# Kernel tuning notes

Measured on AMD Instinct MI355X. Metric: run time of the kernel, lower is better.

## Reference

```python
import jax, jax.numpy as jnp
import numpy as np

NUM_HEADS = 4
EMBED_DIM = 256
HEAD_DIM = EMBED_DIM // NUM_HEADS
B, N = 4, 4096


def setup_inputs() -> dict:
    key = jax.random.key(0)
    kq, kk, kv, kw = jax.random.split(key, 4)
    q = jax.random.normal(kq, (B, N, EMBED_DIM), dtype=jnp.float32)
    k = jax.random.normal(kk, (B, N, EMBED_DIM), dtype=jnp.float32)
    v = jax.random.normal(kv, (B, N, EMBED_DIM), dtype=jnp.float32)
    W_out = jax.random.normal(kw, (EMBED_DIM, EMBED_DIM), dtype=jnp.float32) * (1.0 / np.sqrt(EMBED_DIM))
    b_out = jnp.zeros((EMBED_DIM,), dtype=jnp.float32)
    return {"q": q, "k": k, "v": v, "W_out": W_out, "b_out": b_out}


def reference(q, k, v, W_out, b_out):
    b, n, _ = q.shape
    # [b, n, e] -> [b, h, n, d]
    qh = q.reshape(b, n, NUM_HEADS, HEAD_DIM).transpose(0, 2, 1, 3)
    kh = k.reshape(b, n, NUM_HEADS, HEAD_DIM).transpose(0, 2, 1, 3)
    vh = v.reshape(b, n, NUM_HEADS, HEAD_DIM).transpose(0, 2, 1, 3)
    scale = 1.0 / jnp.sqrt(jnp.asarray(HEAD_DIM, dtype=qh.dtype))
    # full [b, h, n, n] score matrix, as in the original module
    attn = jnp.einsum('bhqd,bhkd->bhqk', qh, kh) * scale
    attn = jax.nn.softmax(attn, axis=-1)
    out = jnp.einsum('bhqk,bhkd->bhqd', attn, vh)
    out = out.transpose(0, 2, 1, 3).reshape(b, n, EMBED_DIM)
    # nn.Linear: x @ W.T + b
    return out @ W_out.T + b_out
```

## Files before the change

### kernel.cpp

```cpp
#include <hip/hip_runtime.h>
#include <hip/hip_bf16.h>

#define B_ 4
#define H_ 4
#define N_ 4096
#define D_ 64
#define E_ 256
#define KVB 64
#define QBLK 256
#define NT (N_ / KVB)

typedef short short8 __attribute__((ext_vector_type(8)));
typedef float f32x4 __attribute__((ext_vector_type(4)));
typedef float f32x16 __attribute__((ext_vector_type(16)));

__device__ __forceinline__ ushort f2bf(float f) {
  union { float f; unsigned u; } a; a.f = f;
  unsigned r = a.u + 0x7fffu + ((a.u >> 16) & 1u);
  return (ushort)(r >> 16);
}

__device__ __forceinline__ unsigned cvt_pk_bf16(float lo, float hi) {
  unsigned r;
  asm("v_cvt_pk_bf16_f32 %0, %1, %2" : "=v"(r) : "v"(lo), "v"(hi));
  return r;
}

__device__ __forceinline__ void permlane32_swap(unsigned &a, unsigned &b) {
  asm volatile("v_permlane32_swap_b32 %0, %1" : "+v"(a), "+v"(b));
}

__global__ void cast_w_kernel(const float* __restrict__ W, ushort* __restrict__ Wb) {
  int i = blockIdx.x * blockDim.x + threadIdx.x;
  float4 x = ((const float4*)W)[i];
  ushort4 o;
  o.x = f2bf(x.x); o.y = f2bf(x.y); o.z = f2bf(x.z); o.w = f2bf(x.w);
  ((ushort4*)Wb)[i] = o;
}

__global__ void prep_kv(const float* __restrict__ k, const float* __restrict__ v,
                        ushort* __restrict__ Kb, ushort* __restrict__ Vtb) {
  __shared__ float vt[64][65];
  const int gid = blockIdx.x;
  const int bh = gid >> 6, t = gid & 63;
  const int b = bh >> 2, h = bh & 3;
  const int tid = threadIdx.x;
  const int rr = tid >> 4, cc = (tid & 15) * 4;
  const float* kg = k + ((size_t)b * N_ + t * 64) * E_ + h * 64;
  const float* vg = v + ((size_t)b * N_ + t * 64) * E_ + h * 64;
  ushort* ko = Kb + (size_t)gid * 4096;
  ushort* vo = Vtb + (size_t)gid * 4096;
  for (int it = 0; it < 4; ++it) {
    int r = rr + it * 16;
    float4 kx = *(const float4*)(kg + (size_t)r * E_ + cc);
    float4 vx = *(const float4*)(vg + (size_t)r * E_ + cc);
    uint2 kp;
    kp.x = (unsigned)f2bf(kx.x) | ((unsigned)f2bf(kx.y) << 16);
    kp.y = (unsigned)f2bf(kx.z) | ((unsigned)f2bf(kx.w) << 16);
    *(uint2*)(ko + r * 64 + cc) = kp;
    vt[r][cc] = vx.x; vt[r][cc + 1] = vx.y; vt[r][cc + 2] = vx.z; vt[r][cc + 3] = vx.w;
  }
  __syncthreads();
  for (int it = 0; it < 4; ++it) {
    int dr = rr + it * 16;
    uint2 vp;
    vp.x = (unsigned)f2bf(vt[cc][dr]) | ((unsigned)f2bf(vt[cc + 1][dr]) << 16);
    vp.y = (unsigned)f2bf(vt[cc + 2][dr]) | ((unsigned)f2bf(vt[cc + 3][dr]) << 16);
    *(uint2*)(vo + dr * 64 + cc) = vp;
  }
}

__launch_bounds__(512, 2)
__global__ void attn_kernel(const float* __restrict__ q,
                            const ushort* __restrict__ Kb,
                            const ushort* __restrict__ Vtb,
                            ushort* __restrict__ X) {
  __shared__ __attribute__((aligned(16))) ushort Ks[2][4096];
  __shared__ __attribute__((aligned(16))) ushort Vs[2][4096];
  __shared__ float Lb[8][32];

  const int bid = blockIdx.x;
  const int swz = (bid & 7) * 32 + (bid >> 3);
  const int bh = swz >> 4;
  const int qt = swz & 15;
  const int b = bh >> 2, h = bh & 3;
  const int tid = threadIdx.x;
  const int wid = tid >> 6;
  const int lane = tid & 63;
  const int ln = lane & 31;
  const int hi = lane >> 5;

  const int off = tid * 16;
  const int sw = (off & ~127) | ((off & 127) ^ (((off >> 7) & 7) << 4));
  const char* Kg = (const char*)Kb + (size_t)bh * NT * 8192;
  const char* Vg = (const char*)Vtb + (size_t)bh * NT * 8192;

  const float SC = 0.125f * 1.44269504f;
  const int qrow0 = qt * QBLK + wid * 32;
  const float* Qg = q + ((size_t)b * N_ + qrow0 + ln) * E_ + h * D_;
  short8 qf[4];
#pragma unroll
  for (int ks = 0; ks < 4; ++ks) {
    const float* p = Qg + ks * 16 + hi * 8;
    float4 x0 = *(const float4*)(p);
    float4 x1 = *(const float4*)(p + 4);
    short8 f;
    f[0] = (short)f2bf(x0.x * SC); f[1] = (short)f2bf(x0.y * SC);
    f[2] = (short)f2bf(x0.z * SC); f[3] = (short)f2bf(x0.w * SC);
    f[4] = (short)f2bf(x1.x * SC); f[5] = (short)f2bf(x1.y * SC);
    f[6] = (short)f2bf(x1.z * SC); f[7] = (short)f2bf(x1.w * SC);
    qf[ks] = f;
  }

  f32x16 O0 = (f32x16)0.0f, O1 = (f32x16)0.0f;
  float lsum = 0.f;

  {
    uint4 k0 = *(const uint4*)(Kg + off);
    uint4 v0 = *(const uint4*)(Vg + off);
    *(uint4*)((char*)Ks[0] + sw) = k0;
    *(uint4*)((char*)Vs[0] + sw) = v0;
  }
  __syncthreads();
  int cur = 0;

  for (int t = 0; t < NT; ++t) {
    const bool pfn = (t + 1 < NT);
    uint4 rk, rv;
    if (pfn) {
      rk = *(const uint4*)(Kg + (size_t)(t + 1) * 8192 + off);
      rv = *(const uint4*)(Vg + (size_t)(t + 1) * 8192 + off);
    }

    short8 kf[2][4];
#pragma unroll
    for (int nb = 0; nb < 2; ++nb)
#pragma unroll
      for (int ks = 0; ks < 4; ++ks) {
        int kvr = nb * 32 + ln;
        kf[nb][ks] = *(short8*)((char*)Ks[cur] + kvr * 128 +
                                ((ks * 32 + hi * 16) ^ ((kvr & 7) << 4)));
      }

    f32x16 S0 = (f32x16)0.0f, S1 = (f32x16)0.0f;
#pragma unroll
    for (int ks = 0; ks < 4; ++ks) {
      S0 = __builtin_amdgcn_mfma_f32_32x32x16_bf16(kf[0][ks], qf[ks], S0, 0, 0, 0);
      S1 = __builtin_amdgcn_mfma_f32_32x32x16_bf16(kf[1][ks], qf[ks], S1, 0, 0, 0);
    }

    float p[32];
#pragma unroll
    for (int i = 0; i < 16; ++i) {
      p[i]      = __builtin_amdgcn_exp2f(S0[i]);
      p[16 + i] = __builtin_amdgcn_exp2f(S1[i]);
    }
    float ls = 0.f;
#pragma unroll
    for (int i = 0; i < 32; ++i) ls += p[i];
    lsum += ls;

    short8 pa[4];
#pragma unroll
    for (int nb = 0; nb < 2; ++nb)
#pragma unroll
      for (int ksp = 0; ksp < 2; ++ksp) {
        int base = nb * 16 + ksp * 8;
        unsigned w0 = cvt_pk_bf16(p[base + 0], p[base + 1]);
        unsigned w2 = cvt_pk_bf16(p[base + 4], p[base + 5]);
        permlane32_swap(w0, w2);
        unsigned w1 = cvt_pk_bf16(p[base + 2], p[base + 3]);
        unsigned w3 = cvt_pk_bf16(p[base + 6], p[base + 7]);
        permlane32_swap(w1, w3);
        uint4 u; u.x = w0; u.y = w1; u.z = w2; u.w = w3;
        union { uint4 u4; short8 s8; } cv; cv.u4 = u;
        pa[nb * 2 + ksp] = cv.s8;
      }

    if (pfn) {
      *(uint4*)((char*)Ks[cur ^ 1] + sw) = rk;
      *(uint4*)((char*)Vs[cur ^ 1] + sw) = rv;
    }

    short8 vf[2][4];
#pragma unroll
    for (int db = 0; db < 2; ++db)
#pragma unroll
      for (int ks = 0; ks < 4; ++ks) {
        int d = db * 32 + ln;
        vf[db][ks] = *(short8*)((char*)Vs[cur] + d * 128 +
                                ((ks * 32 + hi * 16) ^ ((d & 7) << 4)));
      }

#pragma unroll
    for (int ks = 0; ks < 4; ++ks) {
      O0 = __builtin_amdgcn_mfma_f32_32x32x16_bf16(pa[ks], vf[0][ks], O0, 0, 0, 0);
      O1 = __builtin_amdgcn_mfma_f32_32x32x16_bf16(pa[ks], vf[1][ks], O1, 0, 0, 0);
    }

    __syncthreads();
    cur ^= 1;
  }

  float l = lsum + __shfl_xor(lsum, 32);
  if (lane < 32) Lb[wid][lane] = l;
  asm volatile("" ::: "memory");
  float inv[16];
#pragma unroll
  for (int r = 0; r < 16; ++r)
    inv[r] = 1.0f / Lb[wid][(r & 3) + 8 * (r >> 2) + 4 * hi];

  ushort* Xp = X + ((size_t)b * N_) * E_ + h * D_;
#pragma unroll
  for (int r = 0; r < 16; ++r) {
    int qrow = qrow0 + (r & 3) + 8 * (r >> 2) + 4 * hi;
    Xp[(size_t)qrow * E_ + ln]      = f2bf(O0[r] * inv[r]);
    Xp[(size_t)qrow * E_ + 32 + ln] = f2bf(O1[r] * inv[r]);
  }
}

__launch_bounds__(256, 2)
__global__ void proj_kernel(const ushort* __restrict__ X, const ushort* __restrict__ Wb,
                            const float* __restrict__ bias, float* __restrict__ out) {
  const int m0   = blockIdx.x * 64;
  const int tid  = threadIdx.x;
  const int wid  = tid >> 6;
  const int lane = tid & 63;
  const int g    = lane >> 4;
  const int lr   = lane & 15;
  const int n0   = wid * 64;

  f32x4 acc[4][4];
  for (int mb = 0; mb < 4; ++mb)
    for (int nb = 0; nb < 4; ++nb)
      acc[mb][nb] = (f32x4){0.f, 0.f, 0.f, 0.f};

  for (int k0 = 0; k0 < E_; k0 += 32) {
    short8 af[4], bfr[4];
    for (int mb = 0; mb < 4; ++mb)
      af[mb] = *(const short8*)(X + (size_t)(m0 + mb * 16 + lr) * E_ + k0 + g * 8);
    for (int nb = 0; nb < 4; ++nb)
      bfr[nb] = *(const short8*)(Wb + (size_t)(n0 + nb * 16 + lr) * E_ + k0 + g * 8);
    for (int mb = 0; mb < 4; ++mb)
      for (int nb = 0; nb < 4; ++nb)
        acc[mb][nb] = __builtin_amdgcn_mfma_f32_16x16x32_bf16(af[mb], bfr[nb], acc[mb][nb], 0, 0, 0);
  }

  for (int nb = 0; nb < 4; ++nb) {
    float bv = bias[n0 + nb * 16 + lr];
    for (int mb = 0; mb < 4; ++mb)
      for (int r = 0; r < 4; ++r)
        out[(size_t)(m0 + mb * 16 + g * 4 + r) * E_ + n0 + nb * 16 + lr] = acc[mb][nb][r] + bv;
  }
}

extern "C" void kernel_launch(void* const* d_in, const int* in_sizes, int n_in,
                              void* d_out, int out_size, void* d_ws, size_t ws_size,
                              hipStream_t stream) {
  const float* q    = (const float*)d_in[0];
  const float* k    = (const float*)d_in[1];
  const float* v    = (const float*)d_in[2];
  const float* W    = (const float*)d_in[3];
  const float* bias = (const float*)d_in[4];

  char* ws = (char*)d_ws;
  ushort* X   = (ushort*)ws;
  ushort* Wb  = (ushort*)(ws + 8388608);
  ushort* Kb  = (ushort*)(ws + 8388608 + 131072);
  ushort* Vtb = (ushort*)(ws + 8388608 + 131072 + 8388608);

  cast_w_kernel<<<64, 256, 0, stream>>>(W, Wb);
  prep_kv<<<B_ * H_ * NT, 256, 0, stream>>>(k, v, Kb, Vtb);
  attn_kernel<<<B_ * H_ * (N_ / QBLK), 512, 0, stream>>>(q, Kb, Vtb, X);
  proj_kernel<<<(B_ * N_) / 64, 256, 0, stream>>>(X, Wb, bias, (float*)d_out);
}
```

Before: 110.2 us.

## Pre-arrange K/V in MFMA fragment order and shrink query blocks to 128

```diff
diff --git a/kernel.cpp b/kernel.cpp
--- a/kernel.cpp
+++ b/kernel.cpp
@@ -7,7 +7,7 @@
 #define D_ 64
 #define E_ 256
 #define KVB 64
-#define QBLK 256
+#define QBLK 128
 #define NT (N_ / KVB)
 
 typedef short short8 __attribute__((ext_vector_type(8)));
@@ -18,6 +18,16 @@
   union { float f; unsigned u; } a; a.f = f;
   unsigned r = a.u + 0x7fffu + ((a.u >> 16) & 1u);
   return (ushort)(r >> 16);
+}
+
+__device__ __forceinline__ uint4 pack8(float a0, float a1, float a2, float a3,
+                                       float a4, float a5, float a6, float a7) {
+  uint4 u;
+  u.x = (unsigned)f2bf(a0) | ((unsigned)f2bf(a1) << 16);
+  u.y = (unsigned)f2bf(a2) | ((unsigned)f2bf(a3) << 16);
+  u.z = (unsigned)f2bf(a4) | ((unsigned)f2bf(a5) << 16);
+  u.w = (unsigned)f2bf(a6) | ((unsigned)f2bf(a7) << 16);
+  return u;
 }
 
 __device__ __forceinline__ unsigned cvt_pk_bf16(float lo, float hi) {
@@ -50,39 +60,45 @@
   const float* vg = v + ((size_t)b * N_ + t * 64) * E_ + h * 64;
   ushort* ko = Kb + (size_t)gid * 4096;
   ushort* vo = Vtb + (size_t)gid * 4096;
+
   for (int it = 0; it < 4; ++it) {
     int r = rr + it * 16;
-    float4 kx = *(const float4*)(kg + (size_t)r * E_ + cc);
     float4 vx = *(const float4*)(vg + (size_t)r * E_ + cc);
-    uint2 kp;
-    kp.x = (unsigned)f2bf(kx.x) | ((unsigned)f2bf(kx.y) << 16);
-    kp.y = (unsigned)f2bf(kx.z) | ((unsigned)f2bf(kx.w) << 16);
-    *(uint2*)(ko + r * 64 + cc) = kp;
     vt[r][cc] = vx.x; vt[r][cc + 1] = vx.y; vt[r][cc + 2] = vx.z; vt[r][cc + 3] = vx.w;
   }
   __syncthreads();
-  for (int it = 0; it < 4; ++it) {
-    int dr = rr + it * 16;
-    uint2 vp;
-    vp.x = (unsigned)f2bf(vt[cc][dr]) | ((unsigned)f2bf(vt[cc + 1][dr]) << 16);
-    vp.y = (unsigned)f2bf(vt[cc + 2][dr]) | ((unsigned)f2bf(vt[cc + 3][dr]) << 16);
-    *(uint2*)(vo + dr * 64 + cc) = vp;
-  }
-}
-
-__launch_bounds__(512, 2)
+
+  for (int j = 0; j < 2; ++j) {
+    int u = j * 256 + tid;
+    int frag = u >> 6, l = u & 63;
+    int a = (frag >> 2) * 32 + (l & 31);
+    int c0 = (frag & 3) * 16 + ((l >> 5) & 1) * 8;
+    {
+      const float* p = kg + (size_t)a * E_ + c0;
+      float4 x0 = *(const float4*)(p);
+      float4 x1 = *(const float4*)(p + 4);
+      *(uint4*)(ko + u * 8) = pack8(x0.x, x0.y, x0.z, x0.w, x1.x, x1.y, x1.z, x1.w);
+    }
+    {
+      *(uint4*)(vo + u * 8) = pack8(vt[c0][a], vt[c0 + 1][a], vt[c0 + 2][a], vt[c0 + 3][a],
+                                    vt[c0 + 4][a], vt[c0 + 5][a], vt[c0 + 6][a], vt[c0 + 7][a]);
+    }
+  }
+}
+
+__launch_bounds__(256, 2)
 __global__ void attn_kernel(const float* __restrict__ q,
                             const ushort* __restrict__ Kb,
                             const ushort* __restrict__ Vtb,
                             ushort* __restrict__ X) {
   __shared__ __attribute__((aligned(16))) ushort Ks[2][4096];
   __shared__ __attribute__((aligned(16))) ushort Vs[2][4096];
-  __shared__ float Lb[8][32];
+  __shared__ float Lb[4][32];
 
   const int bid = blockIdx.x;
-  const int swz = (bid & 7) * 32 + (bid >> 3);
-  const int bh = swz >> 4;
-  const int qt = swz & 15;
+  const int swz = (bid & 7) * 64 + (bid >> 3);
+  const int bh = swz >> 5;
+  const int qt = swz & 31;
   const int b = bh >> 2, h = bh & 3;
   const int tid = threadIdx.x;
   const int wid = tid >> 6;
@@ -90,8 +106,6 @@
   const int ln = lane & 31;
   const int hi = lane >> 5;
 
-  const int off = tid * 16;
-  const int sw = (off & ~127) | ((off & 127) ^ (((off >> 7) & 7) << 4));
   const char* Kg = (const char*)Kb + (size_t)bh * NT * 8192;
   const char* Vg = (const char*)Vtb + (size_t)bh * NT * 8192;
 
@@ -116,38 +130,45 @@
   float lsum = 0.f;
 
   {
-    uint4 k0 = *(const uint4*)(Kg + off);
-    uint4 v0 = *(const uint4*)(Vg + off);
-    *(uint4*)((char*)Ks[0] + sw) = k0;
-    *(uint4*)((char*)Vs[0] + sw) = v0;
+    uint4 k0 = *(const uint4*)(Kg + tid * 16);
+    uint4 k1 = *(const uint4*)(Kg + 4096 + tid * 16);
+    uint4 v0 = *(const uint4*)(Vg + tid * 16);
+    uint4 v1 = *(const uint4*)(Vg + 4096 + tid * 16);
+    *(uint4*)((char*)Ks[0] + tid * 16) = k0;
+    *(uint4*)((char*)Ks[0] + 4096 + tid * 16) = k1;
+    *(uint4*)((char*)Vs[0] + tid * 16) = v0;
+    *(uint4*)((char*)Vs[0] + 4096 + tid * 16) = v1;
   }
   __syncthreads();
   int cur = 0;
 
   for (int t = 0; t < NT; ++t) {
     const bool pfn = (t + 1 < NT);
-    uint4 rk, rv;
+    uint4 rk0, rk1, rv0, rv1;
     if (pfn) {
-      rk = *(const uint4*)(Kg + (size_t)(t + 1) * 8192 + off);
-      rv = *(const uint4*)(Vg + (size_t)(t + 1) * 8192 + off);
+      const char* kg = Kg + (size_t)(t + 1) * 8192;
+      const char* vg = Vg + (size_t)(t + 1) * 8192;
+      rk0 = *(const uint4*)(kg + tid * 16);
+      rk1 = *(const uint4*)(kg + 4096 + tid * 16);
+      rv0 = *(const uint4*)(vg + tid * 16);
+      rv1 = *(const uint4*)(vg + 4096 + tid * 16);
     }
 
     short8 kf[2][4];
 #pragma unroll
     for (int nb = 0; nb < 2; ++nb)
 #pragma unroll
-      for (int ks = 0; ks < 4; ++ks) {
-        int kvr = nb * 32 + ln;
-        kf[nb][ks] = *(short8*)((char*)Ks[cur] + kvr * 128 +
-                                ((ks * 32 + hi * 16) ^ ((kvr & 7) << 4)));
-      }
+      for (int ks = 0; ks < 4; ++ks)
+        kf[nb][ks] = *(short8*)((char*)Ks[cur] + (nb * 4 + ks) * 1024 + lane * 16);
 
     f32x16 S0 = (f32x16)0.0f, S1 = (f32x16)0.0f;
+    __builtin_amdgcn_s_setprio(1);
 #pragma unroll
     for (int ks = 0; ks < 4; ++ks) {
       S0 = __builtin_amdgcn_mfma_f32_32x32x16_bf16(kf[0][ks], qf[ks], S0, 0, 0, 0);
       S1 = __builtin_amdgcn_mfma_f32_32x32x16_bf16(kf[1][ks], qf[ks], S1, 0, 0, 0);
     }
+    __builtin_amdgcn_s_setprio(0);
 
     float p[32];
 #pragma unroll
@@ -155,10 +176,16 @@
       p[i]      = __builtin_amdgcn_exp2f(S0[i]);
       p[16 + i] = __builtin_amdgcn_exp2f(S1[i]);
     }
-    float ls = 0.f;
-#pragma unroll
-    for (int i = 0; i < 32; ++i) ls += p[i];
-    lsum += ls;
+    {
+      float s1[16];
+#pragma unroll
+      for (int i = 0; i < 16; ++i) s1[i] = p[2 * i] + p[2 * i + 1];
+#pragma unroll
+      for (int i = 0; i < 8; ++i) s1[i] = s1[2 * i] + s1[2 * i + 1];
+#pragma unroll
+      for (int i = 0; i < 4; ++i) s1[i] = s1[2 * i] + s1[2 * i + 1];
+      lsum += (s1[0] + s1[1]) + (s1[2] + s1[3]);
+    }
 
     short8 pa[4];
 #pragma unroll
@@ -178,25 +205,26 @@
       }
 
     if (pfn) {
-      *(uint4*)((char*)Ks[cur ^ 1] + sw) = rk;
-      *(uint4*)((char*)Vs[cur ^ 1] + sw) = rv;
+      *(uint4*)((char*)Ks[cur ^ 1] + tid * 16) = rk0;
+      *(uint4*)((char*)Ks[cur ^ 1] + 4096 + tid * 16) = rk1;
+      *(uint4*)((char*)Vs[cur ^ 1] + tid * 16) = rv0;
+      *(uint4*)((char*)Vs[cur ^ 1] + 4096 + tid * 16) = rv1;
     }
 
     short8 vf[2][4];
 #pragma unroll
     for (int db = 0; db < 2; ++db)
 #pragma unroll
-      for (int ks = 0; ks < 4; ++ks) {
-        int d = db * 32 + ln;
-        vf[db][ks] = *(short8*)((char*)Vs[cur] + d * 128 +
-                                ((ks * 32 + hi * 16) ^ ((d & 7) << 4)));
-      }
-
+      for (int ks = 0; ks < 4; ++ks)
+        vf[db][ks] = *(short8*)((char*)Vs[cur] + (db * 4 + ks) * 1024 + lane * 16);
+
+    __builtin_amdgcn_s_setprio(1);
 #pragma unroll
     for (int ks = 0; ks < 4; ++ks) {
       O0 = __builtin_amdgcn_mfma_f32_32x32x16_bf16(pa[ks], vf[0][ks], O0, 0, 0, 0);
       O1 = __builtin_amdgcn_mfma_f32_32x32x16_bf16(pa[ks], vf[1][ks], O1, 0, 0, 0);
     }
+    __builtin_amdgcn_s_setprio(0);
 
     __syncthreads();
     cur ^= 1;
@@ -271,6 +299,6 @@
 
   cast_w_kernel<<<64, 256, 0, stream>>>(W, Wb);
   prep_kv<<<B_ * H_ * NT, 256, 0, stream>>>(k, v, Kb, Vtb);
-  attn_kernel<<<B_ * H_ * (N_ / QBLK), 512, 0, stream>>>(q, Kb, Vtb, X);
+  attn_kernel<<<B_ * H_ * (N_ / QBLK), 256, 0, stream>>>(q, Kb, Vtb, X);
   proj_kernel<<<(B_ * N_) / 64, 256, 0, stream>>>(X, Wb, bias, (float*)d_out);
 }
```

Result: no change. 111.6 us (+1.3%).
